# Optimization experiments

Measured on AMD Instinct MI355X. Metric: run time of the kernel, lower is better.

The kernel has to match this reference:

```python
import jax, jax.numpy as jnp
import numpy as np

B, T, DM, DK, TOPK, NGRAM = 8, 4096, 1024, 256, 4, 3


def setup_inputs() -> dict:
    key = jax.random.key(0)
    k0, k1, k2, k3 = jax.random.split(key, 4)
    std = np.sqrt(2.0 / (DM + DK)).astype(np.float32)
    query = jax.random.normal(k0, (B, T, DM), jnp.float32)
    key_t = jax.random.normal(k1, (B, T, DM), jnp.float32)
    wq = jax.random.normal(k2, (DK, DM), jnp.float32) * std
    wk = jax.random.normal(k3, (DK, DM), jnp.float32) * std
    bq = jnp.zeros((DK,), jnp.float32)
    bk = jnp.zeros((DK,), jnp.float32)
    # Structured mask: each query row keeps exactly TOPK consecutive key columns
    # (required by the module's masked_select -> view(batch, -1, topk)).
    starts = np.minimum(np.arange(T), T - TOPK)
    cols = starts[:, None] + np.arange(TOPK)[None, :]  # [T, TOPK], ascending
    m = np.ones((T, T), dtype=bool)
    m[np.arange(T)[:, None], cols] = False  # False = unmasked
    mask = jnp.asarray(m)[None]  # [1, T, T]
    return {"query": query, "key": key_t, "mask": mask,
            "wq": wq, "bq": bq, "wk": wk, "bk": bk,
            "topk": TOPK, "ngram": NGRAM}


def reference(query, key, mask, wq, bq, wk, bk, topk, ngram):
    # Projections (torch Linear: x @ W.T + b)
    q = jnp.einsum('btm,dm->btd', query, wq) + bq  # [B,T,DK]
    k = jnp.einsum('btm,dm->btd', key, wk) + bk    # [B,T,DK]
    attn = jax.nn.sigmoid(jnp.einsum('btd,bsd->bts', q, k) / 256.0)  # [B,T,T]
    # masked_select of the topk unmasked entries per row, in ascending column
    # order (matches torch row-major masked_select). argsort of bool puts
    # False (unmasked) columns first, stably, i.e. in ascending column order.
    idx = jnp.argsort(mask, axis=-1)[..., :topk]           # [Bm,T,topk]
    idx = jnp.broadcast_to(idx, attn.shape[:2] + (topk,))  # [B,T,topk]
    sp = jnp.take_along_axis(attn, idx, axis=-1)           # [B,T,topk]
    Bsz = sp.shape[0]
    tt = topk * topk
    # init block: [B,topk,topk] -> repeat along new axis -> [B,1,topk,topk*topk]
    sp_init = jnp.tile(sp[:, :topk, :][:, :, None, :], (1, 1, topk, 1)).reshape(Bsz, 1, topk, tt)
    # end block: repeat each element topk times along last axis
    sp_end = jnp.tile(sp[:, -topk:, :][..., None], (1, 1, 1, topk)).reshape(Bsz, 1, topk, tt)
    # middle n-gram blocks
    mid = sp[:, topk:-topk, :].reshape(Bsz, -1, topk, ngram - 1, topk)  # [B,G,topk,2,topk]
    before = mid[:, :, :, 0, :]  # [B,G,topk,topk]
    after = mid[:, :, :, 1, :]   # [B,G,topk,topk]
    sm = jnp.einsum('bgti,bgtj->bgtij', before, after).reshape(Bsz, -1, topk, tt)
    score_matrix = jnp.concatenate([sp_init, sm, sp_end], axis=1)  # [B,G+2,topk,tt]
    return score_matrix.sum(axis=-1)  # [B, G+2, topk]
```

## Files before the change

kernel.cpp:

```cpp
#include <hip/hip_runtime.h>
#include <hip/hip_bf16.h>
#include <stdint.h>

#define B_ 8
#define T_ 4096
#define DM_ 1024
#define DK_ 256

typedef __attribute__((ext_vector_type(8))) short short8;
typedef __attribute__((ext_vector_type(4))) float f32x4;
typedef __attribute__((ext_vector_type(4))) unsigned short ushort4v;
typedef __attribute__((ext_vector_type(8))) unsigned short ushort8v;

__device__ inline float bf2f(unsigned short u) {
    union { unsigned int u; float f; } v; v.u = ((unsigned int)u) << 16; return v.f;
}
__device__ inline unsigned short f2bf(float f) {
    __hip_bfloat16 h = __float2bfloat16(f);
    return __builtin_bit_cast(unsigned short, h);
}

__device__ inline void gload_lds16(const void* g, void* l) {
    __builtin_amdgcn_global_load_lds(
        (const __attribute__((address_space(1))) unsigned int*)g,
        (__attribute__((address_space(3))) unsigned int*)l, 16, 0, 0);
}

__global__ __launch_bounds__(256) void convw_kernel(
    const float* __restrict__ Wq, const float* __restrict__ Wk,
    unsigned short* __restrict__ Wpk)
{
    int t = blockIdx.x * 256 + threadIdx.x;
    int lane = t & 63;
    int n    = (t >> 6) & 15;
    int kt   = (t >> 10) & 31;
    int M    = t >> 15;
    const float* W = M ? Wk : Wq;
    int row = n * 16 + (lane & 15);
    int k0  = kt * 32 + (lane >> 4) * 8;
    const float* src = W + (size_t)row * DM_ + k0;
    f32x4 v0 = *(const f32x4*)(src);
    f32x4 v1 = *(const f32x4*)(src + 4);
    ushort8v u;
#pragma unroll
    for (int e = 0; e < 4; ++e) { u[e] = f2bf(v0[e]); u[e + 4] = f2bf(v1[e]); }
    *(ushort8v*)(Wpk + (size_t)t * 8) = u;
}

__global__ __launch_bounds__(512, 2) void proj_kernel(
    const float* __restrict__ Aq, const float* __restrict__ Ak,
    const unsigned short* __restrict__ Wpk,
    const float* __restrict__ bq, const float* __restrict__ bk,
    unsigned short* __restrict__ Oq, unsigned short* __restrict__ Ok)
{
    __shared__ __align__(16) char smem[2][24576];

    const bool isK = (blockIdx.z != 0);
    const float* A = isK ? Ak : Aq;
    const unsigned short* Wp = Wpk + (isK ? (size_t)262144 : 0);
    const float* bias = isK ? bk : bq;
    unsigned short* O = isK ? Ok : Oq;

    const int row0 = blockIdx.x * 128;
    const int tid  = threadIdx.x;
    const int w    = tid >> 6;
    const int lane = tid & 63;
    const int lr   = lane & 15;
    const int lq   = lane >> 4;
    const int wr   = (w >> 2) * 64;
    const int wc   = w & 3;

    const int srow = tid >> 2;
    const int schk = tid & 3;
    const float* Asrc = A + (size_t)(row0 + srow) * DM_ + schk * 8;
    const int awaddr = srow * 64 + ((schk ^ (srow & 3)) << 4);

    f32x4 acc[4][4];
#pragma unroll
    for (int m = 0; m < 4; ++m)
#pragma unroll
        for (int n = 0; n < 4; ++n) acc[m][n] = (f32x4){0.f, 0.f, 0.f, 0.f};

    f32x4 av0, av1;

#define LOADA(KT) { const float* p_ = Asrc + (KT) * 32;            \
                    av0 = *(const f32x4*)(p_);                      \
                    av1 = *(const f32x4*)(p_ + 4); }
#define STAGEW(KT, BUF) {                                           \
    const unsigned short* ws_ = Wp + (size_t)(KT) * 8192;           \
    gload_lds16(ws_ + (size_t)tid * 8,          smem[BUF] + 8192  + tid * 16); \
    gload_lds16(ws_ + (size_t)(tid + 512) * 8,  smem[BUF] + 16384 + tid * 16); }
#define CVTWRITE(BUF) {                                             \
    ushort8v u_;                                                    \
    _Pragma("unroll")                                               \
    for (int e_ = 0; e_ < 4; ++e_) {                                \
        u_[e_]     = f2bf(av0[e_]);                                 \
        u_[e_ + 4] = f2bf(av1[e_]);                                 \
    }                                                               \
    *(ushort8v*)(smem[BUF] + awaddr) = u_; }

    STAGEW(0, 0);
    LOADA(0);
    CVTWRITE(0);
    __syncthreads();

    for (int kt = 0; kt < 32; ++kt) {
        const int cur = kt & 1;
        if (kt < 31) {
            STAGEW(kt + 1, cur ^ 1);
            LOADA(kt + 1);
        }

        const char* As = smem[cur];
        const char* Ws = smem[cur] + 8192;
        __builtin_amdgcn_s_setprio(1);
        short8 bF[4];
#pragma unroll
        for (int n = 0; n < 4; ++n)
            bF[n] = *(const short8*)(Ws + ((wc * 4 + n) << 10) + (lane << 4));
#pragma unroll
        for (int m = 0; m < 4; ++m) {
            const int r = wr + m * 16 + lr;
            short8 aF = *(const short8*)(As + r * 64 + ((lq ^ (lr & 3)) << 4));
#pragma unroll
            for (int n = 0; n < 4; ++n)
                acc[m][n] = __builtin_amdgcn_mfma_f32_16x16x32_bf16(
                    bF[n], aF, acc[m][n], 0, 0, 0);
        }
        __builtin_amdgcn_s_setprio(0);

        if (kt < 31) CVTWRITE(cur ^ 1);
        __syncthreads();
    }
#undef LOADA
#undef STAGEW
#undef CVTWRITE

#pragma unroll
    for (int m = 0; m < 4; ++m) {
        unsigned short* Orow = O + (size_t)(row0 + wr + m * 16 + lr) * DK_;
#pragma unroll
        for (int n = 0; n < 4; ++n) {
            const int col = (wc * 4 + n) * 16 + lq * 4;
            f32x4 bv = *(const f32x4*)(bias + col);
            ushort4v ov;
#pragma unroll
            for (int r4 = 0; r4 < 4; ++r4) ov[r4] = f2bf(acc[m][n][r4] + bv[r4]);
            *(ushort4v*)(Orow + col) = ov;
        }
    }
}

__global__ __launch_bounds__(256) void score_kernel(
    const unsigned short* __restrict__ Q, const unsigned short* __restrict__ K,
    float* __restrict__ out)
{
    constexpr int RS = 264;
    __shared__ unsigned short qs[64 * RS];
    __shared__ unsigned short ks[68 * RS];

    const int t0  = blockIdx.x * 64;
    const int b   = blockIdx.y;
    const int tid = threadIdx.x;

#pragma unroll
    for (int j = 0; j < 8; ++j) {
        int idx = j * 256 + tid;
        int r = idx >> 5, c = idx & 31;
        ushort8v v = *(const ushort8v*)(Q + ((size_t)(b * T_ + t0 + r)) * DK_ + c * 8);
        *(ushort8v*)(qs + r * RS + c * 8) = v;
    }
#pragma unroll
    for (int j = 0; j < 9; ++j) {
        int idx = j * 256 + tid;
        if (idx < 68 * 32) {
            int r = idx >> 5, c = idx & 31;
            int gr = t0 + r; if (gr > T_ - 1) gr = T_ - 1;
            ushort8v v = *(const ushort8v*)(K + ((size_t)(b * T_ + gr)) * DK_ + c * 8);
            *(ushort8v*)(ks + r * RS + c * 8) = v;
        }
    }
    __syncthreads();

    const int tl = tid >> 2;
    const int i  = tid & 3;
    const int t  = t0 + tl;
    int s = t; if (s > T_ - 4) s = T_ - 4;
    const int kl = s - t0 + i;

    const ushort8v* qr = (const ushort8v*)(qs + tl * RS);
    const ushort8v* kr = (const ushort8v*)(ks + kl * RS);
    float acc = 0.f;
#pragma unroll
    for (int d8 = 0; d8 < 32; ++d8) {
        ushort8v a = qr[d8], bb = kr[d8];
#pragma unroll
        for (int e = 0; e < 8; ++e) acc += bf2f(a[e]) * bf2f(bb[e]);
    }
    float sig = 1.0f / (1.0f + __expf(-acc * (1.0f / 256.0f)));
    sig += __shfl_xor(sig, 1);
    sig += __shfl_xor(sig, 2);
    float Snext = __shfl_xor(sig, 4);

    if (i == 0) {
        float* ob = out + (size_t)b * (513 * 4);
        if (t < 4) {
            ob[t] = 4.0f * sig;
        } else if (t >= T_ - 4) {
            ob[512 * 4 + (t - (T_ - 4))] = 4.0f * sig;
        }
        if ((t & 1) == 0 && t >= 4 && t < T_ - 4) {
            int pos = t - 4;
            int g = (pos >> 3) + 1;
            int r = (pos >> 1) & 3;
            ob[g * 4 + r] = sig * Snext;
        }
    }
}

extern "C" void kernel_launch(void* const* d_in, const int* in_sizes, int n_in,
                              void* d_out, int out_size, void* d_ws, size_t ws_size,
                              hipStream_t stream)
{
    const float* query = (const float*)d_in[0];
    const float* key   = (const float*)d_in[1];
    const float* wq = (const float*)d_in[3];
    const float* bq = (const float*)d_in[4];
    const float* wk = (const float*)d_in[5];
    const float* bk = (const float*)d_in[6];
    float* out = (float*)d_out;

    unsigned short* Qb  = (unsigned short*)d_ws;
    unsigned short* Kb  = Qb + (size_t)B_ * T_ * DK_;
    unsigned short* Wpk = Kb + (size_t)B_ * T_ * DK_;

    hipLaunchKernelGGL(convw_kernel, dim3(256), dim3(256), 0, stream, wq, wk, Wpk);

    dim3 g1(B_ * T_ / 128, 1, 2);
    hipLaunchKernelGGL(proj_kernel, g1, dim3(512), 0, stream,
                       query, key, Wpk, bq, bk, Qb, Kb);

    dim3 g2(T_ / 64, B_);
    hipLaunchKernelGGL(score_kernel, g2, dim3(256), 0, stream, Qb, Kb, out);
}
```

Baseline: 85.84 us.

## Halve projection row tile to 64 and raise occupancy with new A LDS layout

The projection GEMM now processes 64 rows per block instead of 128, which doubles the grid. Each wave computes a 2x4 tile of MFMA outputs. The A-tile LDS layout changes to k-chunk-major, filled with 4-float loads per thread, and launch bounds now request 6 blocks per CU, which allows more resident waves. This trades more occupancy and more blocks for less reuse of the W tile per block, so each W byte is staged twice as often.

```diff
diff --git a/kernel.cpp b/kernel.cpp
--- a/kernel.cpp
+++ b/kernel.cpp
@@ -47,13 +47,13 @@
     *(ushort8v*)(Wpk + (size_t)t * 8) = u;
 }
 
-__global__ __launch_bounds__(512, 2) void proj_kernel(
+__global__ __launch_bounds__(512, 6) void proj_kernel(
     const float* __restrict__ Aq, const float* __restrict__ Ak,
     const unsigned short* __restrict__ Wpk,
     const float* __restrict__ bq, const float* __restrict__ bk,
     unsigned short* __restrict__ Oq, unsigned short* __restrict__ Ok)
 {
-    __shared__ __align__(16) char smem[2][24576];
+    __shared__ __align__(16) char smem[2][20480];
 
     const bool isK = (blockIdx.z != 0);
     const float* A = isK ? Ak : Aq;
@@ -61,43 +61,38 @@
     const float* bias = isK ? bk : bq;
     unsigned short* O = isK ? Ok : Oq;
 
-    const int row0 = blockIdx.x * 128;
+    const int row0 = blockIdx.x * 64;
     const int tid  = threadIdx.x;
     const int w    = tid >> 6;
     const int lane = tid & 63;
     const int lr   = lane & 15;
     const int lq   = lane >> 4;
-    const int wr   = (w >> 2) * 64;
+    const int wr   = (w >> 2) * 32;
     const int wc   = w & 3;
 
-    const int srow = tid >> 2;
-    const int schk = tid & 3;
-    const float* Asrc = A + (size_t)(row0 + srow) * DM_ + schk * 8;
-    const int awaddr = srow * 64 + ((schk ^ (srow & 3)) << 4);
-
-    f32x4 acc[4][4];
-#pragma unroll
-    for (int m = 0; m < 4; ++m)
+    const int srow = tid >> 3;
+    const int si   = tid & 7;
+    const float* Asrc = A + (size_t)(row0 + srow) * DM_ + si * 4;
+    const int awaddr = ((si >> 1) << 10) + srow * 16 + (si & 1) * 8;
+
+    f32x4 acc[2][4];
+#pragma unroll
+    for (int m = 0; m < 2; ++m)
 #pragma unroll
         for (int n = 0; n < 4; ++n) acc[m][n] = (f32x4){0.f, 0.f, 0.f, 0.f};
 
-    f32x4 av0, av1;
-
-#define LOADA(KT) { const float* p_ = Asrc + (KT) * 32;            \
-                    av0 = *(const f32x4*)(p_);                      \
-                    av1 = *(const f32x4*)(p_ + 4); }
-#define STAGEW(KT, BUF) {                                           \
-    const unsigned short* ws_ = Wp + (size_t)(KT) * 8192;           \
-    gload_lds16(ws_ + (size_t)tid * 8,          smem[BUF] + 8192  + tid * 16); \
-    gload_lds16(ws_ + (size_t)(tid + 512) * 8,  smem[BUF] + 16384 + tid * 16); }
-#define CVTWRITE(BUF) {                                             \
-    ushort8v u_;                                                    \
-    _Pragma("unroll")                                               \
-    for (int e_ = 0; e_ < 4; ++e_) {                                \
-        u_[e_]     = f2bf(av0[e_]);                                 \
-        u_[e_ + 4] = f2bf(av1[e_]);                                 \
-    }                                                               \
-    *(ushort8v*)(smem[BUF] + awaddr) = u_; }
+    f32x4 av;
+
+#define LOADA(KT)  { av = *(const f32x4*)(Asrc + (KT) * 32); }
+#define STAGEW(KT, BUF) {                                               \
+    const unsigned short* ws_ = Wp + (size_t)(KT) * 8192;               \
+    gload_lds16(ws_ + (size_t)tid * 8,         smem[BUF] + 4096  + tid * 16); \
+    gload_lds16(ws_ + (size_t)(tid + 512) * 8, smem[BUF] + 12288 + tid * 16); }
+#define CVTWRITE(BUF) {                                                 \
+    ushort4v u_;                                                        \
+    _Pragma("unroll")                                                   \
+    for (int e_ = 0; e_ < 4; ++e_) u_[e_] = f2bf(av[e_]);               \
+    *(ushort4v*)(smem[BUF] + awaddr) = u_; }
 
     STAGEW(0, 0);
     LOADA(0);
@@ -112,20 +107,22 @@
         }
 
         const char* As = smem[cur];
-        const char* Ws = smem[cur] + 8192;
+        const char* Ws = smem[cur] + 4096;
+
+        short8 aF[2];
+#pragma unroll
+        for (int m = 0; m < 2; ++m) {
+            const int r = wr + m * 16 + lr;
+            aF[m] = *(const short8*)(As + (lq << 10) + r * 16);
+        }
         __builtin_amdgcn_s_setprio(1);
-        short8 bF[4];
-#pragma unroll
-        for (int n = 0; n < 4; ++n)
-            bF[n] = *(const short8*)(Ws + ((wc * 4 + n) << 10) + (lane << 4));
-#pragma unroll
-        for (int m = 0; m < 4; ++m) {
-            const int r = wr + m * 16 + lr;
-            short8 aF = *(const short8*)(As + r * 64 + ((lq ^ (lr & 3)) << 4));
-#pragma unroll
-            for (int n = 0; n < 4; ++n)
+#pragma unroll
+        for (int n = 0; n < 4; ++n) {
+            short8 bF = *(const short8*)(Ws + ((wc * 4 + n) << 10) + (lane << 4));
+#pragma unroll
+            for (int m = 0; m < 2; ++m)
                 acc[m][n] = __builtin_amdgcn_mfma_f32_16x16x32_bf16(
-                    bF[n], aF, acc[m][n], 0, 0, 0);
+                    bF, aF[m], acc[m][n], 0, 0, 0);
         }
         __builtin_amdgcn_s_setprio(0);
 
@@ -137,7 +134,7 @@
 #undef CVTWRITE
 
 #pragma unroll
-    for (int m = 0; m < 4; ++m) {
+    for (int m = 0; m < 2; ++m) {
         unsigned short* Orow = O + (size_t)(row0 + wr + m * 16 + lr) * DK_;
 #pragma unroll
         for (int n = 0; n < 4; ++n) {
@@ -236,7 +233,7 @@
 
     hipLaunchKernelGGL(convw_kernel, dim3(256), dim3(256), 0, stream, wq, wk, Wpk);
 
-    dim3 g1(B_ * T_ / 128, 1, 2);
+    dim3 g1(B_ * T_ / 64, 1, 2);
     hipLaunchKernelGGL(proj_kernel, g1, dim3(512), 0, stream,
                        query, key, Wpk, bq, bk, Qb, Kb);
 
```

After: 105.1 us. +22.5%, slower.
